# Performance work log

Measured on AMD Instinct MI355X. Metric: run time of the kernel, lower is better.

The kernel has to match this reference:

```python
import jax, jax.numpy as jnp
import numpy as np

ALPHA = 0.25
GAMMA = 2.0
LOG_CLAMP = -100.0  # torch binary_cross_entropy clamps log terms at -100


def _conv_same(x, k, stride):
    # x: NHWC, k: HWIO, TF-style SAME padding
    return jax.lax.conv_general_dilated(
        x, k, window_strides=(stride, stride), padding='SAME',
        dimension_numbers=('NHWC', 'HWIO', 'NHWC'))


def _interp_axis(x, axis, out_size):
    # 1-D linear interpolation with align_corners=True semantics
    in_size = x.shape[axis]
    scale = (in_size - 1) / max(out_size - 1, 1)
    pos = jnp.arange(out_size, dtype=x.dtype) * jnp.asarray(scale, dtype=x.dtype)
    i0 = jnp.floor(pos).astype(jnp.int32)
    i1 = jnp.minimum(i0 + 1, in_size - 1)
    w = pos - i0.astype(x.dtype)
    bshape = [1] * x.ndim
    bshape[axis] = out_size
    w = w.reshape(bshape)
    return jnp.take(x, i0, axis=axis) * (1 - w) + jnp.take(x, i1, axis=axis) * w


def _upsample_bilinear_ac(x, factor):
    # NHWC bilinear upsample, align_corners=True (separable)
    x = _interp_axis(x, 1, x.shape[1] * factor)
    x = _interp_axis(x, 2, x.shape[2] * factor)
    return x


def _focal_loss_sum(p, t):
    # binary_cross_entropy (probabilities, not logits) with torch's -100 log clamp
    log_p = jnp.maximum(jnp.log(p), LOG_CLAMP)
    log_1mp = jnp.maximum(jnp.log(1.0 - p), LOG_CLAMP)
    ce = -(t * log_p + (1.0 - t) * log_1mp)
    p_t = p * t + (1.0 - p) * (1.0 - t)
    alpha_t = ALPHA * t + (1.0 - ALPHA) * (1.0 - t)
    return jnp.sum(alpha_t * ce * (1.0 - p_t) ** GAMMA)


def setup_inputs() -> dict:
    key = jax.random.key(0)
    k1, k2 = jax.random.split(key)
    B, H, W = 32, 512, 512
    network_output = jax.random.uniform(k1, (B, H, W, 1), dtype=jnp.float32)
    targets = jax.random.normal(k2, (B, H, W, 2), dtype=jnp.float32)
    # buffers (constants in the original module)
    lap2d = jnp.array([[-1.0, -1.0, -1.0], [-1.0, 8.0, -1.0], [-1.0, -1.0, -1.0]],
                      dtype=jnp.float32)
    laplacian = jnp.stack((lap2d, lap2d), axis=-1).reshape(3, 3, 2, 1)  # HWIO
    fuse_kernel = jnp.array([0.6, 0.3, 0.1], dtype=jnp.float32).reshape(1, 1, 3, 1)
    return {"network_output": network_output, "targets": targets,
            "laplacian": laplacian, "fuse_kernel": fuse_kernel}


def reference(network_output, targets, laplacian, fuse_kernel):
    t = targets[..., 0:2]                                   # [B,H,W,2]
    dt = t.dtype

    b1 = jnp.clip(_conv_same(t, laplacian, 1), 0.0, 1.0)    # [B,H,W,1]
    b1 = (b1 > 0.1).astype(dt)

    b2 = jnp.clip(_conv_same(t, laplacian, 2), 0.0, 1.0)    # [B,H/2,W/2,1]
    b2 = (_upsample_bilinear_ac(b2, 2) > 0.1).astype(dt)

    b4 = jnp.clip(_conv_same(t, laplacian, 4), 0.0, 1.0)    # [B,H/4,W/4,1]
    b4 = (_upsample_bilinear_ac(b4, 4) > 0.1).astype(dt)

    pyr = jnp.concatenate((b1, b2, b4), axis=-1)            # [B,H,W,3]
    fused = _conv_same(pyr, fuse_kernel, 1)                  # [B,H,W,1]
    fused = (fused > 0.1).astype(dt)

    return _focal_loss_sum(network_output, fused)
```

## Files before the change

kernel.cpp:

```cpp
#include <hip/hip_runtime.h>
#include <math.h>


#define B_ 32
#define H_ 512
#define W_ 512

constexpr int TY = 32;
constexpr int TX = 64;
constexpr int RRY = 37;
constexpr int RRX = 69;
constexpr int SSTR = 70;

__global__ __launch_bounds__(256, 8) void edge_focal_kernel(
    const float* __restrict__ net,
    const float* __restrict__ tgt,
    double* __restrict__ partial)
{
    __shared__ float sT[RRY * SSTR];
    __shared__ float sB2[18 * 36];
    __shared__ double sRed[4];

    const int tid = threadIdx.x;
    const int x0 = blockIdx.x * TX;
    const int y0 = blockIdx.y * TY;
    const int b  = blockIdx.z;

    const float* tb = tgt + (size_t)b * (H_ * W_ * 2);
    for (int idx = tid; idx < RRY * 35; idx += 256) {
        int r  = idx / 35;
        int c2 = idx - r * 35;
        int gy = y0 - 2 + r;
        int gx = x0 - 2 + 2 * c2;
        float v0 = 0.f, v1 = 0.f;
        if ((unsigned)gy < (unsigned)H_) {
            if (gx >= 0 && gx + 1 < W_) {
                const float4 q = *reinterpret_cast<const float4*>(tb + ((size_t)gy * W_ + gx) * 2);
                v0 = q.x + q.y; v1 = q.z + q.w;
            } else {
                if ((unsigned)gx < (unsigned)W_) {
                    const float2 t2 = *reinterpret_cast<const float2*>(tb + ((size_t)gy * W_ + gx) * 2);
                    v0 = t2.x + t2.y;
                }
                if ((unsigned)(gx + 1) < (unsigned)W_) {
                    const float2 t2 = *reinterpret_cast<const float2*>(tb + ((size_t)gy * W_ + gx + 1) * 2);
                    v1 = t2.x + t2.y;
                }
            }
        }
        sT[r * SSTR + 2 * c2]     = v0;
        sT[r * SSTR + 2 * c2 + 1] = v1;
    }
    __syncthreads();

    const float s2 = (float)(255.0 / 511.0);

    const int r2lo = (int)((float)y0 * s2);
    const int c2lo = (int)((float)x0 * s2);
    const int r2hi = min((int)((float)(y0 + TY - 1) * s2) + 1, 255);
    const int c2hi = min((int)((float)(x0 + TX - 1) * s2) + 1, 255);
    const int n2r = r2hi - r2lo + 1, n2c = c2hi - c2lo + 1;

    for (int idx = tid; idx < 18 * 36; idx += 256) {
        int rr = idx / 36, cc = idx - rr * 36;
        if (rr < n2r && cc < n2c) {
            int ly = 2 * (r2lo + rr) - (y0 - 2);
            int lx = 2 * (c2lo + cc) - (x0 - 2);
            const float* q0 = &sT[ly * SSTR + lx];
            const float* q1 = q0 + SSTR;
            const float* q2 = q1 + SSTR;
            float s9 = q0[0] + q0[1] + q0[2] + q1[0] + q1[1] + q1[2] + q2[0] + q2[1] + q2[2];
            float cv = 9.f * q1[1] - s9;
            sB2[idx] = fminf(fmaxf(cv, 0.f), 1.f);
        }
    }
    __syncthreads();

    const float* nb = net + (size_t)b * (H_ * W_);
    const int lane = tid & 63;
    const int wv   = tid >> 6;
    const int py0  = wv * 8;
    const int gx   = x0 + lane;
    const int lx   = lane + 2;

    const float posx = (float)gx * s2;
    const int   j0   = (int)posx;
    const int   j1   = min(j0 + 1, 255);
    const float wx   = posx - (float)j0;
    const int   bc0  = j0 - c2lo, bc1 = j1 - c2lo;

    float p[8];
    #pragma unroll
    for (int i = 0; i < 8; ++i)
        p[i] = nb[(size_t)(y0 + py0 + i) * W_ + gx];

    const float* row = &sT[(py0 + 1) * SSTR + lx - 1];
    float rs_m = row[0] + row[1] + row[2];
    row += SSTR;
    float c_c = row[1];
    float rs_c = row[0] + c_c + row[2];

    float facc = 0.f;
    #pragma unroll
    for (int i = 0; i < 8; ++i) {
        const int py = py0 + i;
        const int gy = y0 + py;
        row = &sT[(py + 3) * SSTR + lx - 1];
        const float n0 = row[0], n1 = row[1], n2 = row[2];
        const float rs_p = n0 + n1 + n2;

        const float cv1 = 9.f * c_c - (rs_m + rs_c + rs_p);
        const bool e1 = cv1 > 0.1f;

        const float posy = (float)gy * s2;
        const int   i0   = (int)posy;
        const int   i1   = min(i0 + 1, 255);
        const float wy   = posy - (float)i0;
        const int   a0   = i0 - r2lo, a1 = i1 - r2lo;
        const float v00 = sB2[a0 * 36 + bc0], v01 = sB2[a0 * 36 + bc1];
        const float v10 = sB2[a1 * 36 + bc0], v11 = sB2[a1 * 36 + bc1];
        const float ta  = v00 * (1.f - wy) + v10 * wy;
        const float tb2 = v01 * (1.f - wy) + v11 * wy;
        const float v2  = ta * (1.f - wx) + tb2 * wx;
        const bool e2 = v2 > 0.1f;

        const bool pos = e1 || e2;
        const float pv = p[i];
        const float q  = pos ? pv : 1.f - pv;
        const float al = pos ? 0.25f : 0.75f;
        const float lg = fmaxf(logf(q), -100.f);
        const float om = 1.f - q;
        facc += al * (-lg) * (om * om);

        rs_m = rs_c; rs_c = rs_p; c_c = n1;
    }

    #pragma unroll
    for (int off = 32; off > 0; off >>= 1)
        facc += __shfl_down(facc, off);
    if (lane == 0) sRed[wv] = (double)facc;
    __syncthreads();
    if (tid == 0) {
        partial[((size_t)blockIdx.z * gridDim.y + blockIdx.y) * gridDim.x + blockIdx.x] =
            sRed[0] + sRed[1] + sRed[2] + sRed[3];
    }
}

__global__ __launch_bounds__(256) void reduce_partials(
    const double* __restrict__ partial, float* __restrict__ out, int n)
{
    __shared__ double sRed[4];
    double s = 0.0;
    for (int i = threadIdx.x; i < n; i += 256) s += partial[i];
    #pragma unroll
    for (int off = 32; off > 0; off >>= 1)
        s += __shfl_down(s, off);
    if ((threadIdx.x & 63) == 0) sRed[threadIdx.x >> 6] = s;
    __syncthreads();
    if (threadIdx.x == 0) out[0] = (float)(sRed[0] + sRed[1] + sRed[2] + sRed[3]);
}

extern "C" void kernel_launch(void* const* d_in, const int* in_sizes, int n_in,
                              void* d_out, int out_size, void* d_ws, size_t ws_size,
                              hipStream_t stream) {
    const float* net = (const float*)d_in[0];
    const float* tgt = (const float*)d_in[1];
    double* partial = (double*)d_ws;
    float* out = (float*)d_out;

    const dim3 grid(W_ / TX, H_ / TY, B_);
    hipLaunchKernelGGL(edge_focal_kernel, grid, dim3(256), 0, stream, net, tgt, partial);
    hipLaunchKernelGGL(reduce_partials, dim3(1), dim3(256), 0, stream,
                       partial, out, (int)(grid.x * grid.y * grid.z));
}
```

Before: 129.8 us.

## Hoist net loads, add interior fast path, use fast log, widen final reduce

Moves the per-thread network_output loads to the start of the kernel so their latency overlaps the target tile load and the stride-2 Laplacian stage. Adds a branch-free interior path for tiles whose halo lies fully inside the image, skipping the per-element bounds checks. Replaces logf with the faster, less accurate __logf intrinsic, and widens the single-block partial reduction from 256 to 1024 threads. The earlier loads hold 8 more registers across the shared-memory stages, which may matter under the 8-blocks-per-CU launch bound, and __logf may shift the sum slightly.

```diff
diff --git a/kernel.cpp b/kernel.cpp
--- a/kernel.cpp
+++ b/kernel.cpp
@@ -9,7 +9,6 @@
 constexpr int TY = 32;
 constexpr int TX = 64;
 constexpr int RRY = 37;
-constexpr int RRX = 69;
 constexpr int SSTR = 70;
 
 __global__ __launch_bounds__(256, 8) void edge_focal_kernel(
@@ -26,30 +25,54 @@
     const int y0 = blockIdx.y * TY;
     const int b  = blockIdx.z;
 
+    const int lane = tid & 63;
+    const int wv   = tid >> 6;
+    const int py0  = wv * 8;
+    const int gx   = x0 + lane;
+
+    const float* nb = net + (size_t)b * (H_ * W_);
+    float p[8];
+    #pragma unroll
+    for (int i = 0; i < 8; ++i)
+        p[i] = nb[(size_t)(y0 + py0 + i) * W_ + gx];
+
     const float* tb = tgt + (size_t)b * (H_ * W_ * 2);
-    for (int idx = tid; idx < RRY * 35; idx += 256) {
-        int r  = idx / 35;
-        int c2 = idx - r * 35;
-        int gy = y0 - 2 + r;
-        int gx = x0 - 2 + 2 * c2;
-        float v0 = 0.f, v1 = 0.f;
-        if ((unsigned)gy < (unsigned)H_) {
-            if (gx >= 0 && gx + 1 < W_) {
-                const float4 q = *reinterpret_cast<const float4*>(tb + ((size_t)gy * W_ + gx) * 2);
-                v0 = q.x + q.y; v1 = q.z + q.w;
-            } else {
-                if ((unsigned)gx < (unsigned)W_) {
-                    const float2 t2 = *reinterpret_cast<const float2*>(tb + ((size_t)gy * W_ + gx) * 2);
-                    v0 = t2.x + t2.y;
-                }
-                if ((unsigned)(gx + 1) < (unsigned)W_) {
-                    const float2 t2 = *reinterpret_cast<const float2*>(tb + ((size_t)gy * W_ + gx + 1) * 2);
-                    v1 = t2.x + t2.y;
+    const bool interior = (x0 >= 64) && (x0 <= 384) && (y0 >= 32) && (y0 <= 448);
+    if (interior) {
+        for (int idx = tid; idx < RRY * 35; idx += 256) {
+            int r  = idx / 35;
+            int c2 = idx - r * 35;
+            int gy  = y0 - 2 + r;
+            int gxx = x0 - 2 + 2 * c2;
+            const float4 q = *reinterpret_cast<const float4*>(tb + ((size_t)gy * W_ + gxx) * 2);
+            sT[r * SSTR + 2 * c2]     = q.x + q.y;
+            sT[r * SSTR + 2 * c2 + 1] = q.z + q.w;
+        }
+    } else {
+        for (int idx = tid; idx < RRY * 35; idx += 256) {
+            int r  = idx / 35;
+            int c2 = idx - r * 35;
+            int gy  = y0 - 2 + r;
+            int gxx = x0 - 2 + 2 * c2;
+            float v0 = 0.f, v1 = 0.f;
+            if ((unsigned)gy < (unsigned)H_) {
+                if (gxx >= 0 && gxx + 1 < W_) {
+                    const float4 q = *reinterpret_cast<const float4*>(tb + ((size_t)gy * W_ + gxx) * 2);
+                    v0 = q.x + q.y; v1 = q.z + q.w;
+                } else {
+                    if ((unsigned)gxx < (unsigned)W_) {
+                        const float2 t2 = *reinterpret_cast<const float2*>(tb + ((size_t)gy * W_ + gxx) * 2);
+                        v0 = t2.x + t2.y;
+                    }
+                    if ((unsigned)(gxx + 1) < (unsigned)W_) {
+                        const float2 t2 = *reinterpret_cast<const float2*>(tb + ((size_t)gy * W_ + gxx + 1) * 2);
+                        v1 = t2.x + t2.y;
+                    }
                 }
             }
+            sT[r * SSTR + 2 * c2]     = v0;
+            sT[r * SSTR + 2 * c2 + 1] = v1;
         }
-        sT[r * SSTR + 2 * c2]     = v0;
-        sT[r * SSTR + 2 * c2 + 1] = v1;
     }
     __syncthreads();
 
@@ -76,23 +99,13 @@
     }
     __syncthreads();
 
-    const float* nb = net + (size_t)b * (H_ * W_);
-    const int lane = tid & 63;
-    const int wv   = tid >> 6;
-    const int py0  = wv * 8;
-    const int gx   = x0 + lane;
-    const int lx   = lane + 2;
+    const int lx = lane + 2;
 
     const float posx = (float)gx * s2;
     const int   j0   = (int)posx;
     const int   j1   = min(j0 + 1, 255);
     const float wx   = posx - (float)j0;
     const int   bc0  = j0 - c2lo, bc1 = j1 - c2lo;
-
-    float p[8];
-    #pragma unroll
-    for (int i = 0; i < 8; ++i)
-        p[i] = nb[(size_t)(y0 + py0 + i) * W_ + gx];
 
     const float* row = &sT[(py0 + 1) * SSTR + lx - 1];
     float rs_m = row[0] + row[1] + row[2];
@@ -128,7 +141,7 @@
         const float pv = p[i];
         const float q  = pos ? pv : 1.f - pv;
         const float al = pos ? 0.25f : 0.75f;
-        const float lg = fmaxf(logf(q), -100.f);
+        const float lg = fmaxf(__logf(q), -100.f);
         const float om = 1.f - q;
         facc += al * (-lg) * (om * om);
 
@@ -146,18 +159,23 @@
     }
 }
 
-__global__ __launch_bounds__(256) void reduce_partials(
+__global__ __launch_bounds__(1024) void reduce_partials(
     const double* __restrict__ partial, float* __restrict__ out, int n)
 {
-    __shared__ double sRed[4];
+    __shared__ double sRed[16];
     double s = 0.0;
-    for (int i = threadIdx.x; i < n; i += 256) s += partial[i];
+    for (int i = threadIdx.x; i < n; i += 1024) s += partial[i];
     #pragma unroll
     for (int off = 32; off > 0; off >>= 1)
         s += __shfl_down(s, off);
     if ((threadIdx.x & 63) == 0) sRed[threadIdx.x >> 6] = s;
     __syncthreads();
-    if (threadIdx.x == 0) out[0] = (float)(sRed[0] + sRed[1] + sRed[2] + sRed[3]);
+    if (threadIdx.x == 0) {
+        double t = 0.0;
+        #pragma unroll
+        for (int k = 0; k < 16; ++k) t += sRed[k];
+        out[0] = (float)t;
+    }
 }
 
 extern "C" void kernel_launch(void* const* d_in, const int* in_sizes, int n_in,
@@ -170,6 +188,6 @@
 
     const dim3 grid(W_ / TX, H_ / TY, B_);
     hipLaunchKernelGGL(edge_focal_kernel, grid, dim3(256), 0, stream, net, tgt, partial);
-    hipLaunchKernelGGL(reduce_partials, dim3(1), dim3(256), 0, stream,
+    hipLaunchKernelGGL(reduce_partials, dim3(1), dim3(1024), 0, stream,
                        partial, out, (int)(grid.x * grid.y * grid.z));
 }
```

Result: no change. 130.2 us (+0.3%).
